# Optimization experiments

Hardware: AMD Instinct MI355X
Metric: run time of the kernel (lower is better)

The kernel has to match this reference:

```python
import jax, jax.numpy as jnp
import numpy as np

C = 128          # hidden_channels
N = 100000       # num nodes
E = 500000       # num edges
BN_EPS = 1e-5    # BatchNorm eps (training mode: batch statistics)


def _bn_relu(x, g, b):
    # BatchNorm1d (training mode, biased variance) followed by ReLU
    mu = x.mean(axis=0)
    var = x.var(axis=0)
    return jax.nn.relu(g * (x - mu) * jax.lax.rsqrt(var + BN_EPS) + b)


def setup_inputs() -> dict:
    key = jax.random.key(0)
    ks = jax.random.split(key, 10)
    f = lambda k, s: jax.random.normal(k, s, dtype=jnp.float32) * 0.05
    return {
        "node_rep": f(ks[0], (N, C)),
        "edge_rep": f(ks[1], (E, C)),
        "endpoints": jax.random.randint(ks[2], (2, E), 0, N, dtype=jnp.int64)
            if jax.config.jax_enable_x64 else jax.random.randint(ks[2], (2, E), 0, N, dtype=jnp.int32),
        # lvl_mlp_1: Linear(2C -> C, no bias) + BN(C)
        "W_lvl1": f(ks[3], (2 * C, C)),
        "g_lvl1": jnp.ones((C,), jnp.float32), "b_lvl1": jnp.zeros((C,), jnp.float32),
        # lvl_mlp_2: Linear(C->2C) + BN(2C) + ReLU + Linear(2C->C) + BN(C) + ReLU
        "W_n1": f(ks[4], (C, 2 * C)),
        "g_n1": jnp.ones((2 * C,), jnp.float32), "b_n1": jnp.zeros((2 * C,), jnp.float32),
        "W_n2": f(ks[5], (2 * C, C)),
        "g_n2": jnp.ones((C,), jnp.float32), "b_n2": jnp.zeros((C,), jnp.float32),
        # lift_mlp: Linear(C->2C) + BN(2C) + ReLU + Linear(2C->C) + BN(C) + ReLU
        "W_e1": f(ks[6], (C, 2 * C)),
        "g_e1": jnp.ones((2 * C,), jnp.float32), "b_e1": jnp.zeros((2 * C,), jnp.float32),
        "W_e2": f(ks[7], (2 * C, C)),
        "g_e2": jnp.ones((C,), jnp.float32), "b_e2": jnp.zeros((C,), jnp.float32),
        "eps1": jnp.zeros((), jnp.float32),
        "eps2": jnp.zeros((), jnp.float32),
    }


def reference(node_rep, edge_rep, endpoints,
              W_lvl1, g_lvl1, b_lvl1,
              W_n1, g_n1, b_n1, W_n2, g_n2, b_n2,
              W_e1, g_e1, b_e1, W_e2, g_e2, b_e2,
              eps1, eps2):
    s, t = endpoints[0], endpoints[1]
    # transfer0_0 node->edge: each edge sums its two endpoint node features
    lift_aggr = node_rep[s] + node_rep[t]                       # [E, C]
    h = _bn_relu(jnp.concatenate([lift_aggr, edge_rep], -1) @ W_lvl1,
                 g_lvl1, b_lvl1)                                # [E, C]
    # reverse transfer edge->node: scatter-add to both endpoints
    lvl_aggr = jnp.zeros_like(node_rep).at[s].add(h).at[t].add(h)  # [N, C]
    node_in = (1.0 + eps1) * node_rep + lvl_aggr
    node_out = _bn_relu(_bn_relu(node_in @ W_n1, g_n1, b_n1) @ W_n2, g_n2, b_n2)
    edge_in = (1.0 + eps2) * edge_rep + lift_aggr
    edge_out = _bn_relu(_bn_relu(edge_in @ W_e1, g_e1, b_e1) @ W_e2, g_e2, b_e2)
    return (node_out, edge_out)
```

## Files before the change

kernel.cpp:

```cpp
#include <hip/hip_runtime.h>

#define NN 100000
#define NE 500000

typedef short v8s __attribute__((ext_vector_type(8)));
typedef float v4f __attribute__((ext_vector_type(4)));

__device__ __forceinline__ unsigned short f2bf(float f) {
    unsigned u = __float_as_uint(f);
    u += 0x7fffu + ((u >> 16) & 1u);
    return (unsigned short)(u >> 16);
}
__device__ __forceinline__ float bf2f(unsigned short h) {
    return __uint_as_float(((unsigned)h) << 16);
}
__device__ __forceinline__ unsigned pk2(float a, float b) {
    return (unsigned)f2bf(a) | ((unsigned)f2bf(b) << 16);
}
__device__ __forceinline__ float lo16(unsigned v) { return bf2f((unsigned short)(v & 0xffffu)); }
__device__ __forceinline__ float hi16(unsigned v) { return bf2f((unsigned short)(v >> 16)); }

__device__ __forceinline__ unsigned load2(const void* base, long row, int lane, int f) {
    if (f) return ((const unsigned*)base)[row * 64 + lane];
    const float2 v = ((const float2*)base)[row * 64 + lane];
    return pk2(v.x, v.y);
}

__global__ void detect_k(const unsigned short* __restrict__ edgeR, int* __restrict__ flag) {
    __shared__ int cnt;
    const int tid = threadIdx.x;
    if (tid == 0) cnt = 0;
    __syncthreads();
    const float v = fabsf(bf2f(edgeR[2 * tid]));
    const int sane = (v > 1e-5f && v < 100.f) ? 1 : 0;
    atomicAdd(&cnt, sane);
    __syncthreads();
    if (tid == 0) *flag = (cnt >= 128) ? 1 : 0;
}

__global__ __launch_bounds__(256) void hist_k(const int* __restrict__ ep, int* __restrict__ deg) {
    const int i = blockIdx.x * 256 + threadIdx.x;
    if (i < 2 * NE) atomicAdd(&deg[ep[i]], 1);
}

__global__ __launch_bounds__(1024) void scan_k(int* __restrict__ degcur, int* __restrict__ rowptr) {
    __shared__ int sd[1024];
    const int t = threadIdx.x;
    const int base = t * 98;
    int sum = 0;
    for (int i = 0; i < 98; ++i) {
        const int idx = base + i;
        if (idx < NN) sum += degcur[idx];
    }
    sd[t] = sum;
    __syncthreads();
    for (int off = 1; off < 1024; off <<= 1) {
        const int v = (t >= off) ? sd[t - off] : 0;
        __syncthreads();
        sd[t] += v;
        __syncthreads();
    }
    int run = sd[t] - sum;
    for (int i = 0; i < 98; ++i) {
        const int idx = base + i;
        if (idx < NN) {
            const int d = degcur[idx];
            rowptr[idx] = run;
            degcur[idx] = run;
            run += d;
        }
    }
    if (t == 0) rowptr[NN] = 2 * NE;
}

__global__ __launch_bounds__(256) void fill_k(const int* __restrict__ ep,
                                              int* __restrict__ cursor, int* __restrict__ csr) {
    const int i = blockIdx.x * 256 + threadIdx.x;
    if (i >= 2 * NE) return;
    const int n = ep[i];
    const int pos = atomicAdd(&cursor[n], 1);
    csr[pos] = (i < NE) ? i : (i - NE);
}

__global__ __launch_bounds__(256) void pack_weights(
    const void* __restrict__ W1, const void* __restrict__ Wn1,
    const void* __restrict__ Wn2, const void* __restrict__ We1,
    const void* __restrict__ We2, unsigned short* __restrict__ wpk,
    const int* __restrict__ flag)
{
    const int i = blockIdx.x * 256 + threadIdx.x;
    if (i >= 163840) return;
    const void* W; int Nn; int li = i;
    if (i < 32768)       { W = W1;  Nn = 128; }
    else if (i < 65536)  { W = Wn1; Nn = 256; li -= 32768; }
    else if (i < 98304)  { W = Wn2; Nn = 128; li -= 65536; }
    else if (i < 131072) { W = We1; Nn = 256; li -= 98304; }
    else                 { W = We2; Nn = 128; li -= 131072; }
    const int ntn = Nn >> 4;
    const int j = li & 7, l = (li >> 3) & 63, tile = li >> 9;
    const int ct = tile % ntn, kt = tile / ntn;
    const int k = kt * 32 + (l >> 4) * 8 + j;
    const int n = ct * 16 + (l & 15);
    const int idx = k * Nn + n;
    wpk[i] = (*flag) ? ((const unsigned short*)W)[idx]
                     : f2bf(((const float*)W)[idx]);
}

__global__ __launch_bounds__(256) void kernel_A(
    const void* __restrict__ node, const void* __restrict__ edge,
    const int* __restrict__ ep,
    const unsigned short* __restrict__ wpk1, const unsigned short* __restrict__ wpkE1,
    unsigned short* __restrict__ y1, unsigned short* __restrict__ w1,
    float* __restrict__ stats, const void* __restrict__ eps2p, const int* __restrict__ flag)
{
    __shared__ unsigned short X[64][264];
    const int tid = threadIdx.x, wid = tid >> 6, lane = tid & 63;
    const int mrow = lane & 15, quad = lane >> 4;
    const long e0 = (long)blockIdx.x * 64;
    const int bin = blockIdx.x & 7;
    const int f = *flag;

    for (int rr = 0; rr < 16; ++rr) {
        const int r = wid * 16 + rr;
        const long e = e0 + r;
        unsigned lp = 0, epk = 0;
        if (e < NE) {
            const int s = ep[e], t = ep[NE + e];
            const unsigned a = load2(node, s, lane, f);
            const unsigned b = load2(node, t, lane, f);
            epk = load2(edge, e, lane, f);
            lp = pk2(lo16(a) + lo16(b), hi16(a) + hi16(b));
        }
        *(unsigned*)&X[r][2 * lane] = lp;
        *(unsigned*)&X[r][128 + 2 * lane] = epk;
    }
    __syncthreads();

    {
        v4f acc[4][2];
        #pragma unroll
        for (int rb = 0; rb < 4; ++rb)
            #pragma unroll
            for (int c = 0; c < 2; ++c)
                acc[rb][c] = (v4f){0.f, 0.f, 0.f, 0.f};
        const int ct0 = wid * 2;
        #pragma unroll
        for (int kt = 0; kt < 8; ++kt) {
            v8s a[4];
            #pragma unroll
            for (int rb = 0; rb < 4; ++rb)
                a[rb] = *(const v8s*)&X[rb * 16 + mrow][kt * 32 + quad * 8];
            #pragma unroll
            for (int c = 0; c < 2; ++c) {
                const v8s b = ((const v8s*)wpk1)[(kt * 8 + ct0 + c) * 64 + lane];
                #pragma unroll
                for (int rb = 0; rb < 4; ++rb)
                    acc[rb][c] = __builtin_amdgcn_mfma_f32_16x16x32_bf16(a[rb], b, acc[rb][c], 0, 0, 0);
            }
        }
        #pragma unroll
        for (int c = 0; c < 2; ++c) {
            const int col = (ct0 + c) * 16 + mrow;
            float sy = 0.f, sq = 0.f;
            #pragma unroll
            for (int rb = 0; rb < 4; ++rb) {
                #pragma unroll
                for (int r4 = 0; r4 < 4; ++r4) {
                    const float v = acc[rb][c][r4];
                    const long e = e0 + rb * 16 + quad * 4 + r4;
                    if (e < NE) y1[e * 128 + col] = f2bf(v);
                    sy += v; sq += v * v;
                }
            }
            sy += __shfl_xor(sy, 16); sy += __shfl_xor(sy, 32);
            sq += __shfl_xor(sq, 16); sq += __shfl_xor(sq, 32);
            if (quad == 0) {
                atomicAdd(&stats[bin * 1792 + col], sy);
                atomicAdd(&stats[bin * 1792 + 128 + col], sq);
            }
        }
    }
    __syncthreads();

    const float e2 = 1.f + (f ? bf2f(((const unsigned short*)eps2p)[0])
                              : ((const float*)eps2p)[0]);
    for (int rr = 0; rr < 16; ++rr) {
        const int r = wid * 16 + rr;
        const unsigned lp = *(const unsigned*)&X[r][2 * lane];
        const unsigned ee = *(const unsigned*)&X[r][128 + 2 * lane];
        *(unsigned*)&X[r][2 * lane] = pk2(fmaf(e2, lo16(ee), lo16(lp)),
                                          fmaf(e2, hi16(ee), hi16(lp)));
    }
    __syncthreads();

    {
        v4f acc[4][4];
        #pragma unroll
        for (int rb = 0; rb < 4; ++rb)
            #pragma unroll
            for (int c = 0; c < 4; ++c)
                acc[rb][c] = (v4f){0.f, 0.f, 0.f, 0.f};
        const int ct0 = wid * 4;
        #pragma unroll
        for (int kt = 0; kt < 4; ++kt) {
            v8s a[4];
            #pragma unroll
            for (int rb = 0; rb < 4; ++rb)
                a[rb] = *(const v8s*)&X[rb * 16 + mrow][kt * 32 + quad * 8];
            #pragma unroll
            for (int c = 0; c < 4; ++c) {
                const v8s b = ((const v8s*)wpkE1)[(kt * 16 + ct0 + c) * 64 + lane];
                #pragma unroll
                for (int rb = 0; rb < 4; ++rb)
                    acc[rb][c] = __builtin_amdgcn_mfma_f32_16x16x32_bf16(a[rb], b, acc[rb][c], 0, 0, 0);
            }
        }
        #pragma unroll
        for (int c = 0; c < 4; ++c) {
            const int col = (ct0 + c) * 16 + mrow;
            float sy = 0.f, sq = 0.f;
            #pragma unroll
            for (int rb = 0; rb < 4; ++rb) {
                #pragma unroll
                for (int r4 = 0; r4 < 4; ++r4) {
                    const float v = acc[rb][c][r4];
                    const long e = e0 + rb * 16 + quad * 4 + r4;
                    if (e < NE) w1[e * 256 + col] = f2bf(v);
                    sy += v; sq += v * v;
                }
            }
            sy += __shfl_xor(sy, 16); sy += __shfl_xor(sy, 32);
            sq += __shfl_xor(sq, 16); sq += __shfl_xor(sq, 32);
            if (quad == 0) {
                atomicAdd(&stats[bin * 1792 + 256 + col], sy);
                atomicAdd(&stats[bin * 1792 + 512 + col], sq);
            }
        }
    }
}

__global__ void finalize_k(const float* __restrict__ stats, float* __restrict__ ab,
                           const void* __restrict__ g, const void* __restrict__ bb,
                           const int sOff, const int qOff, const int aOff, const int bOff,
                           const int n, const float invc, const int* __restrict__ flag)
{
    const int c = threadIdx.x;
    if (c >= n) return;
    float S = 0.f, Q = 0.f;
    for (int b = 0; b < 8; ++b) { S += stats[b * 1792 + sOff + c]; Q += stats[b * 1792 + qOff + c]; }
    const float mu = S * invc;
    const float var = Q * invc - mu * mu;
    const float gv = (*flag) ? bf2f(((const unsigned short*)g)[c]) : ((const float*)g)[c];
    const float bv = (*flag) ? bf2f(((const unsigned short*)bb)[c]) : ((const float*)bb)[c];
    const float a = gv * rsqrtf(var + 1e-5f);
    ab[aOff + c] = a;
    ab[bOff + c] = bv - a * mu;
}

__global__ __launch_bounds__(256) void gemm_node1(
    const void* __restrict__ node, const unsigned short* __restrict__ y1,
    const int* __restrict__ rowptr, const int* __restrict__ csr,
    const unsigned short* __restrict__ wpk, unsigned short* __restrict__ z1,
    float* __restrict__ sS, float* __restrict__ sQ,
    const void* __restrict__ eps1p, const float* __restrict__ ab,
    const int* __restrict__ flag)
{
    __shared__ unsigned short X[64][136];
    const int tid = threadIdx.x, wid = tid >> 6, lane = tid & 63;
    const int mrow = lane & 15, quad = lane >> 4;
    const long r0 = (long)blockIdx.x * 64;
    const int bin = blockIdx.x & 7;
    const int f = *flag;
    const float ea = 1.f + (f ? bf2f(((const unsigned short*)eps1p)[0])
                              : ((const float*)eps1p)[0]);
    const int c0 = 2 * lane;
    const float a0 = ab[c0], a1 = ab[c0 + 1];
    const float b0 = ab[128 + c0], b1 = ab[128 + c0 + 1];

    for (int rr = 0; rr < 16; ++rr) {
        const int r = wid * 16 + rr;
        const long gr = r0 + r;
        unsigned o = 0;
        if (gr < NN) {
            float s0 = 0.f, s1 = 0.f;
            const int beg = rowptr[gr], end = rowptr[gr + 1];
            for (int i = beg; i < end; ++i) {
                const int e = csr[i];
                const unsigned v = ((const unsigned*)y1)[(size_t)e * 64 + lane];
                s0 += fmaxf(fmaf(a0, lo16(v), b0), 0.f);
                s1 += fmaxf(fmaf(a1, hi16(v), b1), 0.f);
            }
            const unsigned nr = load2(node, gr, lane, f);
            o = pk2(fmaf(ea, lo16(nr), s0), fmaf(ea, hi16(nr), s1));
        }
        *(unsigned*)&X[r][2 * lane] = o;
    }
    __syncthreads();

    v4f acc[4][4];
    #pragma unroll
    for (int rb = 0; rb < 4; ++rb)
        #pragma unroll
        for (int c = 0; c < 4; ++c)
            acc[rb][c] = (v4f){0.f, 0.f, 0.f, 0.f};
    const int ct0 = wid * 4;
    #pragma unroll
    for (int kt = 0; kt < 4; ++kt) {
        v8s a[4];
        #pragma unroll
        for (int rb = 0; rb < 4; ++rb)
            a[rb] = *(const v8s*)&X[rb * 16 + mrow][kt * 32 + quad * 8];
        #pragma unroll
        for (int c = 0; c < 4; ++c) {
            const v8s b = ((const v8s*)wpk)[(kt * 16 + ct0 + c) * 64 + lane];
            #pragma unroll
            for (int rb = 0; rb < 4; ++rb)
                acc[rb][c] = __builtin_amdgcn_mfma_f32_16x16x32_bf16(a[rb], b, acc[rb][c], 0, 0, 0);
        }
    }
    #pragma unroll
    for (int c = 0; c < 4; ++c) {
        const int col = (ct0 + c) * 16 + mrow;
        float sy = 0.f, sq = 0.f;
        #pragma unroll
        for (int rb = 0; rb < 4; ++rb) {
            #pragma unroll
            for (int r4 = 0; r4 < 4; ++r4) {
                const float v = acc[rb][c][r4];
                const long gr = r0 + rb * 16 + quad * 4 + r4;
                if (gr < NN) z1[gr * 256 + col] = f2bf(v);
                sy += v; sq += v * v;
            }
        }
        sy += __shfl_xor(sy, 16); sy += __shfl_xor(sy, 32);
        sq += __shfl_xor(sq, 16); sq += __shfl_xor(sq, 32);
        if (quad == 0) {
            atomicAdd(&sS[bin * 1792 + col], sy);
            atomicAdd(&sQ[bin * 1792 + col], sq);
        }
    }
}

__global__ __launch_bounds__(256) void gemm_k256(
    const unsigned short* __restrict__ in, const float* __restrict__ aab,
    const float* __restrict__ bab, const unsigned short* __restrict__ wpk,
    unsigned short* __restrict__ out, float* __restrict__ sS, float* __restrict__ sQ,
    const long rows)
{
    __shared__ unsigned short X[64][264];
    const int tid = threadIdx.x, wid = tid >> 6, lane = tid & 63;
    const int mrow = lane & 15, quad = lane >> 4;
    const long r0 = (long)blockIdx.x * 64;
    const int bin = blockIdx.x & 7;
    const float4 av = ((const float4*)aab)[lane];
    const float4 bv = ((const float4*)bab)[lane];
    for (int rr = 0; rr < 16; ++rr) {
        const int r = wid * 16 + rr;
        const long gr = r0 + r;
        ushort4 o = {0, 0, 0, 0};
        if (gr < rows) {
            const ushort4 w = *(const ushort4*)(in + gr * 256 + 4 * lane);
            o.x = f2bf(fmaxf(fmaf(av.x, bf2f(w.x), bv.x), 0.f));
            o.y = f2bf(fmaxf(fmaf(av.y, bf2f(w.y), bv.y), 0.f));
            o.z = f2bf(fmaxf(fmaf(av.z, bf2f(w.z), bv.z), 0.f));
            o.w = f2bf(fmaxf(fmaf(av.w, bf2f(w.w), bv.w), 0.f));
        }
        *(ushort4*)&X[r][4 * lane] = o;
    }
    __syncthreads();
    v4f acc[4][2];
    #pragma unroll
    for (int rb = 0; rb < 4; ++rb)
        #pragma unroll
        for (int c = 0; c < 2; ++c)
            acc[rb][c] = (v4f){0.f, 0.f, 0.f, 0.f};
    const int ct0 = wid * 2;
    #pragma unroll
    for (int kt = 0; kt < 8; ++kt) {
        v8s a[4];
        #pragma unroll
        for (int rb = 0; rb < 4; ++rb)
            a[rb] = *(const v8s*)&X[rb * 16 + mrow][kt * 32 + quad * 8];
        #pragma unroll
        for (int c = 0; c < 2; ++c) {
            const v8s b = ((const v8s*)wpk)[(kt * 8 + ct0 + c) * 64 + lane];
            #pragma unroll
            for (int rb = 0; rb < 4; ++rb)
                acc[rb][c] = __builtin_amdgcn_mfma_f32_16x16x32_bf16(a[rb], b, acc[rb][c], 0, 0, 0);
        }
    }
    #pragma unroll
    for (int c = 0; c < 2; ++c) {
        const int col = (ct0 + c) * 16 + mrow;
        float sy = 0.f, sq = 0.f;
        #pragma unroll
        for (int rb = 0; rb < 4; ++rb) {
            #pragma unroll
            for (int r4 = 0; r4 < 4; ++r4) {
                const float v = acc[rb][c][r4];
                const long gr = r0 + rb * 16 + quad * 4 + r4;
                if (gr < rows) out[gr * 128 + col] = f2bf(v);
                sy += v; sq += v * v;
            }
        }
        sy += __shfl_xor(sy, 16); sy += __shfl_xor(sy, 32);
        sq += __shfl_xor(sq, 16); sq += __shfl_xor(sq, 32);
        if (quad == 0) {
            atomicAdd(&sS[bin * 1792 + col], sy);
            atomicAdd(&sQ[bin * 1792 + col], sq);
        }
    }
}

__global__ __launch_bounds__(256) void final_k(
    const unsigned short* __restrict__ z2, const unsigned short* __restrict__ w2,
    const float* __restrict__ ab, void* __restrict__ out, const int* __restrict__ flag)
{
    const long p = (long)blockIdx.x * 256 + threadIdx.x;
    const long npn = (long)NN * 64;
    const long tot = npn + (long)NE * 64;
    if (p >= tot) return;
    long el, oe; const unsigned short* src; int abA, abB;
    if (p < npn) { el = p * 2; oe = el; src = z2; abA = 1536; abB = 1664; }
    else { el = (p - npn) * 2; oe = (long)NN * 128 + el; src = w2; abA = 1280; abB = 1408; }
    const int col = (int)(el & 127);
    const unsigned v = *(const unsigned*)(src + el);
    const float o0 = fmaxf(fmaf(ab[abA + col], lo16(v), ab[abB + col]), 0.f);
    const float o1 = fmaxf(fmaf(ab[abA + col + 1], hi16(v), ab[abB + col + 1]), 0.f);
    if (*flag) {
        *(unsigned*)((unsigned short*)out + oe) = pk2(o0, o1);
    } else {
        float2 f; f.x = o0; f.y = o1;
        *(float2*)((float*)out + oe) = f;
    }
}

extern "C" void kernel_launch(void* const* d_in, const int* in_sizes, int n_in,
                              void* d_out, int out_size, void* d_ws, size_t ws_size,
                              hipStream_t stream)
{
    (void)in_sizes; (void)n_in; (void)out_size; (void)ws_size;
    const unsigned short* edgeR = (const unsigned short*)d_in[1];
    const int* ep = (const int*)d_in[2];

    char* ws = (char*)d_ws;
    unsigned short* wpk = (unsigned short*)ws;
    float* stats   = (float*)(ws + 327680);
    float* ab      = (float*)(ws + 385024);
    int*   flag    = (int*)(ws + 392192);
    int*   rowptr  = (int*)(ws + 392448);
    int*   cursor  = (int*)(ws + 792576);
    int*   csr     = (int*)(ws + 1192704);
    unsigned short* y1 = (unsigned short*)(ws + 5192704);
    unsigned short* w1 = (unsigned short*)(ws + 133192704);
    unsigned short* w2 = (unsigned short*)(ws + 389192704);
    unsigned short* z1 = (unsigned short*)(ws + 517192704);
    unsigned short* z2 = (unsigned short*)(ws + 568392704);

    const unsigned short* wpk1  = wpk;
    const unsigned short* wpkN1 = wpk + 32768;
    const unsigned short* wpkN2 = wpk + 65536;
    const unsigned short* wpkE1 = wpk + 98304;
    const unsigned short* wpkE2 = wpk + 131072;

    detect_k<<<1, 256, 0, stream>>>(edgeR, flag);
    hipMemsetAsync(stats, 0, 57344, stream);
    hipMemsetAsync(cursor, 0, 400000, stream);

    hist_k<<<3907, 256, 0, stream>>>(ep, cursor);
    scan_k<<<1, 1024, 0, stream>>>(cursor, rowptr);
    fill_k<<<3907, 256, 0, stream>>>(ep, cursor, csr);

    pack_weights<<<640, 256, 0, stream>>>(d_in[3], d_in[6], d_in[9], d_in[12], d_in[15], wpk, flag);

    kernel_A<<<7813, 256, 0, stream>>>(d_in[0], d_in[1], ep, wpk1, wpkE1, y1, w1, stats, d_in[19], flag);
    finalize_k<<<1, 128, 0, stream>>>(stats, ab, d_in[4], d_in[5], 0, 128, 0, 128, 128, 1.f / NE, flag);
    finalize_k<<<1, 256, 0, stream>>>(stats, ab, d_in[13], d_in[14], 256, 512, 256, 512, 256, 1.f / NE, flag);

    gemm_node1<<<1563, 256, 0, stream>>>(d_in[0], y1, rowptr, csr, wpkN1, z1,
                                         stats + 768, stats + 1024, d_in[18], ab, flag);
    finalize_k<<<1, 256, 0, stream>>>(stats, ab, d_in[7], d_in[8], 768, 1024, 768, 1024, 256, 1.f / NN, flag);

    gemm_k256<<<1563, 256, 0, stream>>>(z1, ab + 768, ab + 1024, wpkN2, z2,
                                        stats + 1536, stats + 1664, (long)NN);
    finalize_k<<<1, 128, 0, stream>>>(stats, ab, d_in[10], d_in[11], 1536, 1664, 1536, 1664, 128, 1.f / NN, flag);

    gemm_k256<<<7813, 256, 0, stream>>>(w1, ab + 256, ab + 512, wpkE2, w2,
                                        stats + 1280, stats + 1408, (long)NE);
    finalize_k<<<1, 128, 0, stream>>>(stats, ab, d_in[16], d_in[17], 1280, 1408, 1280, 1408, 128, 1.f / NE, flag);

    final_k<<<150000, 256, 0, stream>>>(z2, w2, ab, d_out, flag);
}
```

Measured before the change: 2.061 ms.

## Recompute first-layer GEMMs instead of storing 256-wide intermediates, swizzle LDS

The 256-channel hidden activations (w1, z1) are no longer written to memory. The first-stage kernels write only the 128-channel bf16 inputs (edge_in, node_in) and keep the statistics pass. A new fused kernel recomputes the first linear layer, applies BN+ReLU in LDS and runs the second GEMM. This trades extra MFMA work for much less HBM traffic. The change also XOR-swizzles LDS instead of padding, widens the gathers and the final elementwise pass, raises the stats bins to 32 and adds occupancy launch bounds.

New measurement: 1.840 ms. -10.7%, faster.

```diff
diff --git a/kernel.cpp b/kernel.cpp
--- a/kernel.cpp
+++ b/kernel.cpp
@@ -106,33 +106,53 @@
                      : f2bf(((const float*)W)[idx]);
 }
 
-__global__ __launch_bounds__(256) void kernel_A(
+__global__ __launch_bounds__(256, 5) void kernel_A(
     const void* __restrict__ node, const void* __restrict__ edge,
     const int* __restrict__ ep,
     const unsigned short* __restrict__ wpk1, const unsigned short* __restrict__ wpkE1,
-    unsigned short* __restrict__ y1, unsigned short* __restrict__ w1,
+    unsigned short* __restrict__ y1, unsigned short* __restrict__ edge_in,
     float* __restrict__ stats, const void* __restrict__ eps2p, const int* __restrict__ flag)
 {
-    __shared__ unsigned short X[64][264];
+    __shared__ unsigned short X[64 * 256];
     const int tid = threadIdx.x, wid = tid >> 6, lane = tid & 63;
     const int mrow = lane & 15, quad = lane >> 4;
-    const long e0 = (long)blockIdx.x * 64;
-    const int bin = blockIdx.x & 7;
+    const int li = lane & 31, hb = lane >> 5;
+    const int e0 = blockIdx.x * 64;
+    const int e0w = e0 + wid * 16;
+    const int bin = blockIdx.x & 31;
     const int f = *flag;
 
-    for (int rr = 0; rr < 16; ++rr) {
-        const int r = wid * 16 + rr;
-        const long e = e0 + r;
-        unsigned lp = 0, epk = 0;
-        if (e < NE) {
-            const int s = ep[e], t = ep[NE + e];
-            const unsigned a = load2(node, s, lane, f);
-            const unsigned b = load2(node, t, lane, f);
-            epk = load2(edge, e, lane, f);
-            lp = pk2(lo16(a) + lo16(b), hi16(a) + hi16(b));
-        }
-        *(unsigned*)&X[r][2 * lane] = lp;
-        *(unsigned*)&X[r][128 + 2 * lane] = epk;
+    const int ei = e0w + mrow;
+    int sv = 0, tv = 0;
+    if (ei < NE) { sv = ep[ei]; tv = ep[NE + ei]; }
+
+    #pragma unroll
+    for (int j = 0; j < 8; ++j) {
+        const int eA = e0w + 2 * j + hb;
+        const int s = __shfl(sv, 2 * j + hb);
+        const int t = __shfl(tv, 2 * j + hb);
+        uint2 lp = {0u, 0u}, ee = {0u, 0u};
+        if (eA < NE) {
+            if (f) {
+                const uint2 a = ((const uint2*)node)[s * 32 + li];
+                const uint2 b = ((const uint2*)node)[t * 32 + li];
+                ee = ((const uint2*)edge)[(size_t)eA * 32 + li];
+                lp.x = pk2(lo16(a.x) + lo16(b.x), hi16(a.x) + hi16(b.x));
+                lp.y = pk2(lo16(a.y) + lo16(b.y), hi16(a.y) + hi16(b.y));
+            } else {
+                const float4 a = ((const float4*)node)[s * 32 + li];
+                const float4 b = ((const float4*)node)[t * 32 + li];
+                const float4 ev = ((const float4*)edge)[(size_t)eA * 32 + li];
+                lp.x = pk2(a.x + b.x, a.y + b.y);
+                lp.y = pk2(a.z + b.z, a.w + b.w);
+                ee.x = pk2(ev.x, ev.y);
+                ee.y = pk2(ev.z, ev.w);
+            }
+        }
+        const int r = wid * 16 + 2 * j + hb;
+        const int swz = (r & 7) << 3;
+        *(uint2*)&X[r * 256 + ((li * 4) ^ swz)] = lp;
+        *(uint2*)&X[r * 256 + ((128 + li * 4) ^ swz)] = ee;
     }
     __syncthreads();
 
@@ -148,8 +168,10 @@
         for (int kt = 0; kt < 8; ++kt) {
             v8s a[4];
             #pragma unroll
-            for (int rb = 0; rb < 4; ++rb)
-                a[rb] = *(const v8s*)&X[rb * 16 + mrow][kt * 32 + quad * 8];
+            for (int rb = 0; rb < 4; ++rb) {
+                const int r = rb * 16 + mrow;
+                a[rb] = *(const v8s*)&X[r * 256 + ((kt * 32 + quad * 8) ^ ((r & 7) << 3))];
+            }
             #pragma unroll
             for (int c = 0; c < 2; ++c) {
                 const v8s b = ((const v8s*)wpk1)[(kt * 8 + ct0 + c) * 64 + lane];
@@ -167,8 +189,8 @@
                 #pragma unroll
                 for (int r4 = 0; r4 < 4; ++r4) {
                     const float v = acc[rb][c][r4];
-                    const long e = e0 + rb * 16 + quad * 4 + r4;
-                    if (e < NE) y1[e * 128 + col] = f2bf(v);
+                    const int e = e0 + rb * 16 + quad * 4 + r4;
+                    if (e < NE) y1[(size_t)e * 128 + col] = f2bf(v);
                     sy += v; sq += v * v;
                 }
             }
@@ -184,12 +206,16 @@
 
     const float e2 = 1.f + (f ? bf2f(((const unsigned short*)eps2p)[0])
                               : ((const float*)eps2p)[0]);
+    #pragma unroll
     for (int rr = 0; rr < 16; ++rr) {
         const int r = wid * 16 + rr;
-        const unsigned lp = *(const unsigned*)&X[r][2 * lane];
-        const unsigned ee = *(const unsigned*)&X[r][128 + 2 * lane];
-        *(unsigned*)&X[r][2 * lane] = pk2(fmaf(e2, lo16(ee), lo16(lp)),
-                                          fmaf(e2, hi16(ee), hi16(lp)));
+        const int swz = (r & 7) << 3;
+        const unsigned lp = *(const unsigned*)&X[r * 256 + ((2 * lane) ^ swz)];
+        const unsigned ee = *(const unsigned*)&X[r * 256 + ((128 + 2 * lane) ^ swz)];
+        const unsigned o = pk2(fmaf(e2, lo16(ee), lo16(lp)), fmaf(e2, hi16(ee), hi16(lp)));
+        *(unsigned*)&X[r * 256 + ((2 * lane) ^ swz)] = o;
+        const int e = e0 + r;
+        if (e < NE) ((unsigned*)edge_in)[(size_t)e * 64 + lane] = o;
     }
     __syncthreads();
 
@@ -205,8 +231,10 @@
         for (int kt = 0; kt < 4; ++kt) {
             v8s a[4];
             #pragma unroll
-            for (int rb = 0; rb < 4; ++rb)
-                a[rb] = *(const v8s*)&X[rb * 16 + mrow][kt * 32 + quad * 8];
+            for (int rb = 0; rb < 4; ++rb) {
+                const int r = rb * 16 + mrow;
+                a[rb] = *(const v8s*)&X[r * 256 + ((kt * 32 + quad * 8) ^ ((r & 7) << 3))];
+            }
             #pragma unroll
             for (int c = 0; c < 4; ++c) {
                 const v8s b = ((const v8s*)wpkE1)[(kt * 16 + ct0 + c) * 64 + lane];
@@ -224,8 +252,6 @@
                 #pragma unroll
                 for (int r4 = 0; r4 < 4; ++r4) {
                     const float v = acc[rb][c][r4];
-                    const long e = e0 + rb * 16 + quad * 4 + r4;
-                    if (e < NE) w1[e * 256 + col] = f2bf(v);
                     sy += v; sq += v * v;
                 }
             }
@@ -247,7 +273,7 @@
     const int c = threadIdx.x;
     if (c >= n) return;
     float S = 0.f, Q = 0.f;
-    for (int b = 0; b < 8; ++b) { S += stats[b * 1792 + sOff + c]; Q += stats[b * 1792 + qOff + c]; }
+    for (int b = 0; b < 32; ++b) { S += stats[b * 1792 + sOff + c]; Q += stats[b * 1792 + qOff + c]; }
     const float mu = S * invc;
     const float var = Q * invc - mu * mu;
     const float gv = (*flag) ? bf2f(((const unsigned short*)g)[c]) : ((const float*)g)[c];
@@ -257,19 +283,19 @@
     ab[bOff + c] = bv - a * mu;
 }
 
-__global__ __launch_bounds__(256) void gemm_node1(
+__global__ __launch_bounds__(256, 5) void gemm_node1(
     const void* __restrict__ node, const unsigned short* __restrict__ y1,
     const int* __restrict__ rowptr, const int* __restrict__ csr,
-    const unsigned short* __restrict__ wpk, unsigned short* __restrict__ z1,
+    const unsigned short* __restrict__ wpk, unsigned short* __restrict__ node_in,
     float* __restrict__ sS, float* __restrict__ sQ,
     const void* __restrict__ eps1p, const float* __restrict__ ab,
     const int* __restrict__ flag)
 {
-    __shared__ unsigned short X[64][136];
+    __shared__ unsigned short X[64 * 128];
     const int tid = threadIdx.x, wid = tid >> 6, lane = tid & 63;
     const int mrow = lane & 15, quad = lane >> 4;
     const long r0 = (long)blockIdx.x * 64;
-    const int bin = blockIdx.x & 7;
+    const int bin = blockIdx.x & 31;
     const int f = *flag;
     const float ea = 1.f + (f ? bf2f(((const unsigned short*)eps1p)[0])
                               : ((const float*)eps1p)[0]);
@@ -293,7 +319,8 @@
             const unsigned nr = load2(node, gr, lane, f);
             o = pk2(fmaf(ea, lo16(nr), s0), fmaf(ea, hi16(nr), s1));
         }
-        *(unsigned*)&X[r][2 * lane] = o;
+        *(unsigned*)&X[r * 128 + ((2 * lane) ^ ((r & 7) << 3))] = o;
+        if (gr < NN) ((unsigned*)node_in)[gr * 64 + lane] = o;
     }
     __syncthreads();
 
@@ -308,8 +335,10 @@
     for (int kt = 0; kt < 4; ++kt) {
         v8s a[4];
         #pragma unroll
-        for (int rb = 0; rb < 4; ++rb)
-            a[rb] = *(const v8s*)&X[rb * 16 + mrow][kt * 32 + quad * 8];
+        for (int rb = 0; rb < 4; ++rb) {
+            const int r = rb * 16 + mrow;
+            a[rb] = *(const v8s*)&X[r * 128 + ((kt * 32 + quad * 8) ^ ((r & 7) << 3))];
+        }
         #pragma unroll
         for (int c = 0; c < 4; ++c) {
             const v8s b = ((const v8s*)wpk)[(kt * 16 + ct0 + c) * 64 + lane];
@@ -327,8 +356,6 @@
             #pragma unroll
             for (int r4 = 0; r4 < 4; ++r4) {
                 const float v = acc[rb][c][r4];
-                const long gr = r0 + rb * 16 + quad * 4 + r4;
-                if (gr < NN) z1[gr * 256 + col] = f2bf(v);
                 sy += v; sq += v * v;
             }
         }
@@ -341,63 +368,100 @@
     }
 }
 
-__global__ __launch_bounds__(256) void gemm_k256(
+__global__ __launch_bounds__(256, 5) void fused2_k(
     const unsigned short* __restrict__ in, const float* __restrict__ aab,
-    const float* __restrict__ bab, const unsigned short* __restrict__ wpk,
-    unsigned short* __restrict__ out, float* __restrict__ sS, float* __restrict__ sQ,
-    const long rows)
-{
-    __shared__ unsigned short X[64][264];
+    const float* __restrict__ bab, const unsigned short* __restrict__ wpkA,
+    const unsigned short* __restrict__ wpkB, unsigned short* __restrict__ out,
+    float* __restrict__ sS, float* __restrict__ sQ, const long rows)
+{
+    __shared__ unsigned short X[64 * 256];
     const int tid = threadIdx.x, wid = tid >> 6, lane = tid & 63;
     const int mrow = lane & 15, quad = lane >> 4;
     const long r0 = (long)blockIdx.x * 64;
-    const int bin = blockIdx.x & 7;
-    const float4 av = ((const float4*)aab)[lane];
-    const float4 bv = ((const float4*)bab)[lane];
-    for (int rr = 0; rr < 16; ++rr) {
-        const int r = wid * 16 + rr;
+    const int bin = blockIdx.x & 31;
+
+    #pragma unroll
+    for (int i = 0; i < 4; ++i) {
+        const int r = wid * 16 + i * 4 + quad;
         const long gr = r0 + r;
-        ushort4 o = {0, 0, 0, 0};
-        if (gr < rows) {
-            const ushort4 w = *(const ushort4*)(in + gr * 256 + 4 * lane);
-            o.x = f2bf(fmaxf(fmaf(av.x, bf2f(w.x), bv.x), 0.f));
-            o.y = f2bf(fmaxf(fmaf(av.y, bf2f(w.y), bv.y), 0.f));
-            o.z = f2bf(fmaxf(fmaf(av.z, bf2f(w.z), bv.z), 0.f));
-            o.w = f2bf(fmaxf(fmaf(av.w, bf2f(w.w), bv.w), 0.f));
-        }
-        *(ushort4*)&X[r][4 * lane] = o;
-    }
-    __syncthreads();
-    v4f acc[4][2];
+        v8s v = (v8s){0, 0, 0, 0, 0, 0, 0, 0};
+        if (gr < rows) v = *(const v8s*)(in + gr * 128 + mrow * 8);
+        *(v8s*)&X[r * 256 + ((mrow * 8) ^ ((r & 7) << 3))] = v;
+    }
+    __syncthreads();
+
+    v4f acc[4][4];
     #pragma unroll
     for (int rb = 0; rb < 4; ++rb)
         #pragma unroll
+        for (int c = 0; c < 4; ++c)
+            acc[rb][c] = (v4f){0.f, 0.f, 0.f, 0.f};
+    const int ct0 = wid * 4;
+    #pragma unroll
+    for (int kt = 0; kt < 4; ++kt) {
+        v8s a[4];
+        #pragma unroll
+        for (int rb = 0; rb < 4; ++rb) {
+            const int r = rb * 16 + mrow;
+            a[rb] = *(const v8s*)&X[r * 256 + ((kt * 32 + quad * 8) ^ ((r & 7) << 3))];
+        }
+        #pragma unroll
+        for (int c = 0; c < 4; ++c) {
+            const v8s b = ((const v8s*)wpkA)[(kt * 16 + ct0 + c) * 64 + lane];
+            #pragma unroll
+            for (int rb = 0; rb < 4; ++rb)
+                acc[rb][c] = __builtin_amdgcn_mfma_f32_16x16x32_bf16(a[rb], b, acc[rb][c], 0, 0, 0);
+        }
+    }
+    __syncthreads();
+
+    #pragma unroll
+    for (int c = 0; c < 4; ++c) {
+        const int col = (ct0 + c) * 16 + mrow;
+        const float av = aab[col], bv = bab[col];
+        #pragma unroll
+        for (int rb = 0; rb < 4; ++rb)
+            #pragma unroll
+            for (int r4 = 0; r4 < 4; ++r4) {
+                const int r = rb * 16 + quad * 4 + r4;
+                const float h = (r0 + r < rows) ? fmaxf(fmaf(av, acc[rb][c][r4], bv), 0.f) : 0.f;
+                X[r * 256 + (col ^ ((r & 7) << 3))] = f2bf(h);
+            }
+    }
+    __syncthreads();
+
+    v4f acc2[4][2];
+    #pragma unroll
+    for (int rb = 0; rb < 4; ++rb)
+        #pragma unroll
         for (int c = 0; c < 2; ++c)
-            acc[rb][c] = (v4f){0.f, 0.f, 0.f, 0.f};
-    const int ct0 = wid * 2;
+            acc2[rb][c] = (v4f){0.f, 0.f, 0.f, 0.f};
+    const int ct2 = wid * 2;
     #pragma unroll
     for (int kt = 0; kt < 8; ++kt) {
         v8s a[4];
         #pragma unroll
-        for (int rb = 0; rb < 4; ++rb)
-            a[rb] = *(const v8s*)&X[rb * 16 + mrow][kt * 32 + quad * 8];
+        for (int rb = 0; rb < 4; ++rb) {
+            const int r = rb * 16 + mrow;
+            a[rb] = *(const v8s*)&X[r * 256 + ((kt * 32 + quad * 8) ^ ((r & 7) << 3))];
+        }
         #pragma unroll
         for (int c = 0; c < 2; ++c) {
-            const v8s b = ((const v8s*)wpk)[(kt * 8 + ct0 + c) * 64 + lane];
+            const v8s b = ((const v8s*)wpkB)[(kt * 8 + ct2 + c) * 64 + lane];
             #pragma unroll
             for (int rb = 0; rb < 4; ++rb)
-                acc[rb][c] = __builtin_amdgcn_mfma_f32_16x16x32_bf16(a[rb], b, acc[rb][c], 0, 0, 0);
+                acc2[rb][c] = __builtin_amdgcn_mfma_f32_16x16x32_bf16(a[rb], b, acc2[rb][c], 0, 0, 0);
         }
     }
     #pragma unroll
     for (int c = 0; c < 2; ++c) {
-        const int col = (ct0 + c) * 16 + mrow;
+        const int col = (ct2 + c) * 16 + mrow;
         float sy = 0.f, sq = 0.f;
         #pragma unroll
         for (int rb = 0; rb < 4; ++rb) {
             #pragma unroll
             for (int r4 = 0; r4 < 4; ++r4) {
-                const float v = acc[rb][c][r4];
+                const float v = acc2[rb][c][r4];
                 const long gr = r0 + rb * 16 + quad * 4 + r4;
                 if (gr < rows) out[gr * 128 + col] = f2bf(v);
                 sy += v; sq += v * v;
@@ -417,21 +481,24 @@
     const float* __restrict__ ab, void* __restrict__ out, const int* __restrict__ flag)
 {
     const long p = (long)blockIdx.x * 256 + threadIdx.x;
-    const long npn = (long)NN * 64;
-    const long tot = npn + (long)NE * 64;
+    const long npn = (long)NN * 32;
+    const long tot = npn + (long)NE * 32;
     if (p >= tot) return;
     long el, oe; const unsigned short* src; int abA, abB;
-    if (p < npn) { el = p * 2; oe = el; src = z2; abA = 1536; abB = 1664; }
-    else { el = (p - npn) * 2; oe = (long)NN * 128 + el; src = w2; abA = 1280; abB = 1408; }
+    if (p < npn) { el = p * 4; oe = el; src = z2; abA = 1536; abB = 1664; }
+    else { el = (p - npn) * 4; oe = (long)NN * 128 + el; src = w2; abA = 1280; abB = 1408; }
     const int col = (int)(el & 127);
-    const unsigned v = *(const unsigned*)(src + el);
-    const float o0 = fmaxf(fmaf(ab[abA + col], lo16(v), ab[abB + col]), 0.f);
-    const float o1 = fmaxf(fmaf(ab[abA + col + 1], hi16(v), ab[abB + col + 1]), 0.f);
+    const uint2 v = *(const uint2*)(src + el);
+    const float o0 = fmaxf(fmaf(ab[abA + col],     lo16(v.x), ab[abB + col]),     0.f);
+    const float o1 = fmaxf(fmaf(ab[abA + col + 1], hi16(v.x), ab[abB + col + 1]), 0.f);
+    const float o2 = fmaxf(fmaf(ab[abA + col + 2], lo16(v.y), ab[abB + col + 2]), 0.f);
+    const float o3 = fmaxf(fmaf(ab[abA + col + 3], hi16(v.y), ab[abB + col + 3]), 0.f);
     if (*flag) {
-        *(unsigned*)((unsigned short*)out + oe) = pk2(o0, o1);
+        uint2 r; r.x = pk2(o0, o1); r.y = pk2(o2, o3);
+        *(uint2*)((unsigned short*)out + oe) = r;
     } else {
-        float2 f; f.x = o0; f.y = o1;
-        *(float2*)((float*)out + oe) = f;
+        float4 f; f.x = o0; f.y = o1; f.z = o2; f.w = o3;
+        *(float4*)((float*)out + oe) = f;
     }
 }
 
@@ -446,16 +513,16 @@
     char* ws = (char*)d_ws;
     unsigned short* wpk = (unsigned short*)ws;
     float* stats   = (float*)(ws + 327680);
-    float* ab      = (float*)(ws + 385024);
-    int*   flag    = (int*)(ws + 392192);
-    int*   rowptr  = (int*)(ws + 392448);
-    int*   cursor  = (int*)(ws + 792576);
-    int*   csr     = (int*)(ws + 1192704);
-    unsigned short* y1 = (unsigned short*)(ws + 5192704);
-    unsigned short* w1 = (unsigned short*)(ws + 133192704);
-    unsigned short* w2 = (unsigned short*)(ws + 389192704);
-    unsigned short* z1 = (unsigned short*)(ws + 517192704);
-    unsigned short* z2 = (unsigned short*)(ws + 568392704);
+    float* ab      = (float*)(ws + 557056);
+    int*   flag    = (int*)(ws + 564224);
+    int*   rowptr  = (int*)(ws + 564480);
+    int*   cursor  = (int*)(ws + 964608);
+    int*   csr     = (int*)(ws + 1364736);
+    unsigned short* y1      = (unsigned short*)(ws + 5364736);
+    unsigned short* edge_in = (unsigned short*)(ws + 133364736);
+    unsigned short* w2      = (unsigned short*)(ws + 261364736);
+    unsigned short* node_in = (unsigned short*)(ws + 389364736);
+    unsigned short* z2      = (unsigned short*)(ws + 414964736);
 
     const unsigned short* wpk1  = wpk;
     const unsigned short* wpkN1 = wpk + 32768;
@@ -464,7 +531,7 @@
     const unsigned short* wpkE2 = wpk + 131072;
 
     detect_k<<<1, 256, 0, stream>>>(edgeR, flag);
-    hipMemsetAsync(stats, 0, 57344, stream);
+    hipMemsetAsync(stats, 0, 229376, stream);
     hipMemsetAsync(cursor, 0, 400000, stream);
 
     hist_k<<<3907, 256, 0, stream>>>(ep, cursor);
@@ -473,21 +540,21 @@
 
     pack_weights<<<640, 256, 0, stream>>>(d_in[3], d_in[6], d_in[9], d_in[12], d_in[15], wpk, flag);
 
-    kernel_A<<<7813, 256, 0, stream>>>(d_in[0], d_in[1], ep, wpk1, wpkE1, y1, w1, stats, d_in[19], flag);
+    kernel_A<<<7813, 256, 0, stream>>>(d_in[0], d_in[1], ep, wpk1, wpkE1, y1, edge_in, stats, d_in[19], flag);
     finalize_k<<<1, 128, 0, stream>>>(stats, ab, d_in[4], d_in[5], 0, 128, 0, 128, 128, 1.f / NE, flag);
     finalize_k<<<1, 256, 0, stream>>>(stats, ab, d_in[13], d_in[14], 256, 512, 256, 512, 256, 1.f / NE, flag);
 
-    gemm_node1<<<1563, 256, 0, stream>>>(d_in[0], y1, rowptr, csr, wpkN1, z1,
+    gemm_node1<<<1563, 256, 0, stream>>>(d_in[0], y1, rowptr, csr, wpkN1, node_in,
                                          stats + 768, stats + 1024, d_in[18], ab, flag);
     finalize_k<<<1, 256, 0, stream>>>(stats, ab, d_in[7], d_in[8], 768, 1024, 768, 1024, 256, 1.f / NN, flag);
 
-    gemm_k256<<<1563, 256, 0, stream>>>(z1, ab + 768, ab + 1024, wpkN2, z2,
-                                        stats + 1536, stats + 1664, (long)NN);
+    fused2_k<<<1563, 256, 0, stream>>>(node_in, ab + 768, ab + 1024, wpkN1, wpkN2, z2,
+                                       stats + 1536, stats + 1664, (long)NN);
     finalize_k<<<1, 128, 0, stream>>>(stats, ab, d_in[10], d_in[11], 1536, 1664, 1536, 1664, 128, 1.f / NN, flag);
 
-    gemm_k256<<<7813, 256, 0, stream>>>(w1, ab + 256, ab + 512, wpkE2, w2,
-                                        stats + 1280, stats + 1408, (long)NE);
+    fused2_k<<<7813, 256, 0, stream>>>(edge_in, ab + 256, ab + 512, wpkE1, wpkE2, w2,
+                                       stats + 1280, stats + 1408, (long)NE);
     finalize_k<<<1, 128, 0, stream>>>(stats, ab, d_in[16], d_in[17], 1280, 1408, 1280, 1408, 128, 1.f / NE, flag);
 
-    final_k<<<150000, 256, 0, stream>>>(z2, w2, ab, d_out, flag);
-}
+    final_k<<<75000, 256, 0, stream>>>(z2, w2, ab, d_out, flag);
+}
```
